# Kernel tuning notes

Hardware: AMD Instinct MI355X
Metric: run time of the kernel (lower is better)

The kernel has to match this reference:

```python
import jax, jax.numpy as jnp
import numpy as np

# Architecture constants pinned by the source script
D_MODEL = 2      # input_size / problemDim
ED = 64          # d_inner = expand_factor * d_model = hidden_size
N = 32           # d_state
K = 16           # d_conv
DT_RANK = 1      # ceil(d_model / 16)
NC = 4           # num_classes
B, L = 16, 2048


def setup_inputs() -> dict:
    key = jax.random.key(0)
    ks = jax.random.split(key, 16)
    rn = lambda k, shape, sc=0.1: jax.random.normal(k, shape, jnp.float32) * sc
    return {
        "x": jax.random.normal(ks[0], (B, L, D_MODEL), jnp.float32),
        "norm_w": jnp.ones((D_MODEL,), jnp.float32),
        "w_in": rn(ks[1], (D_MODEL, 2 * ED)),            # in_proj (no bias)
        "conv_w": rn(ks[2], (ED, 1, K)),                  # depthwise causal conv
        "conv_b": rn(ks[3], (ED,)),
        "w_xproj": rn(ks[4], (ED, DT_RANK + 2 * N)),      # x_proj (no bias)
        "w_dt": rn(ks[5], (DT_RANK, ED)),                 # dt_proj
        "b_dt": rn(ks[6], (ED,)),
        "A_log": jnp.log(jnp.tile(jnp.arange(1, N + 1, dtype=jnp.float32), (ED, 1))),
        "D_skip": jnp.ones((ED,), jnp.float32),
        "w_out": rn(ks[7], (ED, ED)),                     # out_proj (classifier mode: d_inner->d_inner)
        "b_out": rn(ks[8], (ED,)),
        "w_fc": rn(ks[9], (ED, ED)),
        "b_fc": rn(ks[10], (ED,)),
        "w_cls": rn(ks[11], (ED, NC)),
        "b_cls": rn(ks[12], (NC,)),
        "w_reg": rn(ks[13], (ED, 1)),
        "b_reg": rn(ks[14], (1,)),
    }


def _rmsnorm(x, w, eps=1e-5):
    return x * jax.lax.rsqrt(jnp.mean(x * x, axis=-1, keepdims=True) + eps) * w


def _silu(x):
    return x * jax.nn.sigmoid(x)


def reference(x, norm_w, w_in, conv_w, conv_b, w_xproj, w_dt, b_dt, A_log, D_skip,
              w_out, b_out, w_fc, b_fc, w_cls, b_cls, w_reg, b_reg):
    # --- Mamba block (n_layers = 1, classifier mode: no residual back to d_model) ---
    h = _rmsnorm(x, norm_w)                                # [B,L,D]
    xz = h @ w_in                                          # [B,L,2*ED]
    xb, z = jnp.split(xz, 2, axis=-1)
    # depthwise causal conv over time (torch pads K-1 both sides then slices [:L] == left-pad K-1)
    xc = jnp.transpose(xb, (0, 2, 1))                      # [B,ED,L]
    xc = jax.lax.conv_general_dilated(
        xc, conv_w, window_strides=(1,), padding=[(K - 1, 0)],
        feature_group_count=ED, dimension_numbers=("NCH", "OIH", "NCH"))
    xc = xc + conv_b[None, :, None]
    xb = _silu(jnp.transpose(xc, (0, 2, 1)))               # [B,L,ED]
    # input-dependent SSM parameters
    dbc = xb @ w_xproj                                     # [B,L,dt_rank+2N]
    delta = jax.nn.softplus(dbc[..., :DT_RANK] @ w_dt + b_dt)   # [B,L,ED]
    Bm = dbc[..., DT_RANK:DT_RANK + N]                     # [B,L,N]
    C = dbc[..., DT_RANK + N:]                             # [B,L,N]
    A = -jnp.exp(A_log)                                    # [ED,N]
    dA = jnp.exp(delta[..., None] * A)                     # [B,L,ED,N]
    dBx = delta[..., None] * Bm[:, :, None, :] * xb[..., None]  # [B,L,ED,N]

    # selective scan: h_t = dA_t * h_{t-1} + dBx_t ; y_t = <h_t, C_t>
    def step(hst, inp):
        dA_t, dBx_t, C_t = inp
        hst = dA_t * hst + dBx_t                           # [B,ED,N]
        y = jnp.einsum("ben,bn->be", hst, C_t)
        return hst, y

    h0 = jnp.zeros((x.shape[0], ED, N), x.dtype)
    xs = (jnp.transpose(dA, (1, 0, 2, 3)),
          jnp.transpose(dBx, (1, 0, 2, 3)),
          jnp.transpose(C, (1, 0, 2)))
    _, ys = jax.lax.scan(step, h0, xs)                     # [L,B,ED]
    y = jnp.transpose(ys, (1, 0, 2)) + D_skip * xb         # [B,L,ED]
    y = y * _silu(z)                                       # gate
    out = y @ w_out + b_out                                # [B,L,ED]

    last = out[:, -1, :]                                   # [B,ED]
    hs = jax.nn.relu(last @ w_fc + b_fc)
    class_logits = hs @ w_cls + b_cls                      # [B,NC]
    mass_pred = (hs @ w_reg + b_reg)[:, 0]                 # [B]
    return class_logits, mass_pred
```

## Files before the change

### kernel.cpp

```cpp
#include <hip/hip_runtime.h>
#include <math.h>

#define BB 16
#define LL 2048
#define ED 64
#define NN 32
#define KK 16
#define NCHUNK 64
#define CH 32
#define NBLK (BB * NCHUNK)
#define NSEG 4
#define CPS (NCHUNK / NSEG)

__global__ __launch_bounds__(256) void k1_featscan(
    const float* __restrict__ x, const float* __restrict__ norm_w,
    const float* __restrict__ w_in, const float* __restrict__ conv_w,
    const float* __restrict__ conv_b, const float* __restrict__ w_xproj,
    const float* __restrict__ w_dt, const float* __restrict__ b_dt,
    float* __restrict__ sbuf, float* __restrict__ dsumbuf,
    float* __restrict__ xlast, float* __restrict__ zl, float* __restrict__ cl)
{
    const int bx = blockIdx.x;
    const int b = bx >> 6, ti = bx & 63;
    const int l0 = ti * CH;
    const int tid = threadIdx.x;

    __shared__ float xbl[CH][ED + 1];
    __shared__ float hh[2 * (CH + KK - 1)];
    __shared__ float wdt[ED];
    __shared__ float wxs[ED][NN];
    __shared__ float dsp[4][ED];
    __shared__ __align__(16) union U {
        float pre[CH + KK - 1][ED];
        struct {
            float2 dlrl[CH][ED];
            float bml[CH][36];
            float dtr[CH];
        } sb;
    } u;

    for (int idx = tid; idx < ED * NN; idx += 256) {
        int e = idx >> 5, j = idx & 31;
        wxs[e][j] = w_xproj[e * 65 + 1 + j];
    }
    if (tid < ED) wdt[tid] = w_xproj[tid * 65];

    if (tid < 2 * (CH + KK - 1)) {
        int p = tid >> 1, c = tid & 1;
        int l = l0 - (KK - 1) + p;
        hh[tid] = (l >= 0) ? x[(b * LL + l) * 2 + c] : 0.f;
    }
    __syncthreads();
    if (tid < CH + KK - 1) {
        float x0 = hh[2 * tid], x1 = hh[2 * tid + 1];
        float s = rsqrtf(0.5f * (x0 * x0 + x1 * x1) + 1e-5f);
        hh[2 * tid]     = x0 * s * norm_w[0];
        hh[2 * tid + 1] = x1 * s * norm_w[1];
    }
    __syncthreads();
    {
        const int e = tid & 63;
        const float w0 = w_in[e], w1 = w_in[128 + e];
        for (int idx = tid; idx < (CH + KK - 1) * ED; idx += 256) {
            int p = idx >> 6;
            u.pre[p][e] = hh[2 * p] * w0 + hh[2 * p + 1] * w1;
        }
    }
    __syncthreads();
    {
        const int e = tid & 63, tg = tid >> 6, t0 = tg * 8;
        const float4 c0 = *(const float4*)(conv_w + e * KK);
        const float4 c1 = *(const float4*)(conv_w + e * KK + 4);
        const float4 c2 = *(const float4*)(conv_w + e * KK + 8);
        const float4 c3 = *(const float4*)(conv_w + e * KK + 12);
        const float cw[KK] = {c0.x, c0.y, c0.z, c0.w, c1.x, c1.y, c1.z, c1.w,
                              c2.x, c2.y, c2.z, c2.w, c3.x, c3.y, c3.z, c3.w};
        float w[8 + KK - 1];
        #pragma unroll
        for (int i = 0; i < 8 + KK - 1; ++i) w[i] = u.pre[t0 + i][e];
        const float bias = conv_b[e];
        #pragma unroll
        for (int i = 0; i < 8; ++i) {
            float acc = bias;
            #pragma unroll
            for (int k = 0; k < KK; ++k) acc = __fmaf_rn(cw[k], w[i + k], acc);
            xbl[t0 + i][e] = acc / (1.f + __expf(-acc));
        }
    }
    __syncthreads();
    {
        const int t = tid & 31, jg = tid >> 5;
        float a0 = 0.f, a1 = 0.f, a2 = 0.f, a3 = 0.f;
        for (int e = 0; e < ED; ++e) {
            float xv = xbl[t][e];
            const float4 wv = *(const float4*)&wxs[e][jg * 4];
            a0 = __fmaf_rn(xv, wv.x, a0);
            a1 = __fmaf_rn(xv, wv.y, a1);
            a2 = __fmaf_rn(xv, wv.z, a2);
            a3 = __fmaf_rn(xv, wv.w, a3);
        }
        u.sb.bml[t][jg * 4 + 0] = a0;
        u.sb.bml[t][jg * 4 + 1] = a1;
        u.sb.bml[t][jg * 4 + 2] = a2;
        u.sb.bml[t][jg * 4 + 3] = a3;
    }
    if (tid < CH) {
        float acc = 0.f;
        for (int e = 0; e < ED; ++e)
            acc = __fmaf_rn(xbl[tid][e], wdt[e], acc);
        u.sb.dtr[tid] = acc;
    }
    if (ti == NCHUNK - 1) {
        if (tid < NN) {
            float acc = 0.f;
            for (int e = 0; e < ED; ++e)
                acc = __fmaf_rn(xbl[CH - 1][e], w_xproj[e * 65 + 33 + tid], acc);
            cl[b * NN + tid] = acc;
        } else if (tid >= 64 && tid < 128) {
            int e = tid - 64;
            int pl = 2 * (CH + KK - 2);
            zl[b * ED + e] = hh[pl] * w_in[64 + e] + hh[pl + 1] * w_in[192 + e];
        } else if (tid >= 128 && tid < 192) {
            int e = tid - 128;
            xlast[b * ED + e] = xbl[CH - 1][e];
        }
    }
    __syncthreads();
    {
        const int e = tid & 63, tg = tid >> 6;
        const float wde = w_dt[e], bde = b_dt[e];
        float dpart = 0.f;
        #pragma unroll
        for (int k = 0; k < 8; ++k) {
            int s = tg + 4 * k;
            float v = __fmaf_rn(u.sb.dtr[s], wde, bde);
            float d = (v > 15.f) ? v : __logf(1.f + __expf(v));
            dpart += d;
            u.sb.dlrl[s][e] = make_float2(__expf(-d), d * xbl[s][e]);
        }
        dsp[tg][e] = dpart;
    }
    __syncthreads();
    {
        const int e = tid & 63, ng = tid >> 6, n0 = ng * 8;
        float S[8];
        #pragma unroll
        for (int j = 0; j < 8; ++j) S[j] = 0.f;

        for (int s = 0; s < CH; ++s) {
            const float2 rd = u.sb.dlrl[s][e];
            const float r = rd.x, dx = rd.y;
            const float4 b0 = *(const float4*)&u.sb.bml[s][n0];
            const float4 b1 = *(const float4*)&u.sb.bml[s][n0 + 4];
            float r2 = r * r, r4 = r2 * r2, r8 = r4 * r4;
            float bb1 = (ng & 1) ? r8 : 1.f;
            float bb2 = (ng & 2) ? r8 * r8 : 1.f;
            float m = r * bb1 * bb2;
            S[0] = __fmaf_rn(m, S[0], dx * b0.x); m *= r;
            S[1] = __fmaf_rn(m, S[1], dx * b0.y); m *= r;
            S[2] = __fmaf_rn(m, S[2], dx * b0.z); m *= r;
            S[3] = __fmaf_rn(m, S[3], dx * b0.w); m *= r;
            S[4] = __fmaf_rn(m, S[4], dx * b1.x); m *= r;
            S[5] = __fmaf_rn(m, S[5], dx * b1.y); m *= r;
            S[6] = __fmaf_rn(m, S[6], dx * b1.z); m *= r;
            S[7] = __fmaf_rn(m, S[7], dx * b1.w);
        }

        const int gbase = (ti * BB + b) * (ED * NN) + e * NN + n0;
        *(float4*)&sbuf[gbase]     = make_float4(S[0], S[1], S[2], S[3]);
        *(float4*)&sbuf[gbase + 4] = make_float4(S[4], S[5], S[6], S[7]);
        if (tid < 64) {
            float Dsum = dsp[0][tid] + dsp[1][tid] + dsp[2][tid] + dsp[3][tid];
            dsumbuf[(ti * BB + b) * ED + tid] = Dsum;
        }
    }
}

__global__ __launch_bounds__(256) void k2_fold(
    const float* __restrict__ sbuf, const float* __restrict__ dsumbuf,
    const float* __restrict__ A_log, float* __restrict__ hfin)
{
    const int tid = threadIdx.x;
    const int sid = tid & 63, seg = tid >> 6;
    const int state = blockIdx.x * 64 + sid;
    const int b = state >> 11, r = state & 2047;
    const int e = r >> 5, n = r & 31;
    const float A = -__expf(A_log[e * NN + n]);

    float M = 1.f, S = 0.f;
    const int c0 = seg * CPS;
    #pragma unroll
    for (int k = 0; k < CPS; ++k) {
        const int c = c0 + k;
        float m = __expf(A * dsumbuf[(c * BB + b) * ED + e]);
        S = __fmaf_rn(m, S, sbuf[(c * BB + b) * (ED * NN) + r]);
        M *= m;
    }

    __shared__ float Ms[NSEG][64], Ss[NSEG][64];
    Ms[seg][sid] = M;
    Ss[seg][sid] = S;
    __syncthreads();
    if (seg == 0) {
        float h = S;
        #pragma unroll
        for (int k = 1; k < NSEG; ++k)
            h = __fmaf_rn(Ms[k][sid], h, Ss[k][sid]);
        hfin[state] = h;
    }
}

__global__ __launch_bounds__(256) void k3_tail(
    const float* __restrict__ hfin, const float* __restrict__ cl,
    const float* __restrict__ zl, const float* __restrict__ xlast,
    const float* __restrict__ D_skip, const float* __restrict__ w_out,
    const float* __restrict__ b_out, const float* __restrict__ w_fc,
    const float* __restrict__ b_fc, const float* __restrict__ w_cls,
    const float* __restrict__ b_cls, const float* __restrict__ w_reg,
    const float* __restrict__ b_reg, float* __restrict__ out)
{
    const int b = blockIdx.x, tid = threadIdx.x;
    const int e = tid & 63, ng = tid >> 6, n0 = ng * 8;

    __shared__ float part[4][ED];
    __shared__ float ylds[ED], olds[ED], hlds[ED];

    float acc;
    {
        const float4 h0 = *(const float4*)&hfin[b * (ED * NN) + e * NN + n0];
        const float4 h1 = *(const float4*)&hfin[b * (ED * NN) + e * NN + n0 + 4];
        const float4 q0 = *(const float4*)&cl[b * NN + n0];
        const float4 q1 = *(const float4*)&cl[b * NN + n0 + 4];
        acc = h0.x * q0.x + h0.y * q0.y + h0.z * q0.z + h0.w * q0.w
            + h1.x * q1.x + h1.y * q1.y + h1.z * q1.z + h1.w * q1.w;
    }
    part[ng][e] = acc;
    __syncthreads();

    if (tid < ED) {
        float y = part[0][tid] + part[1][tid] + part[2][tid] + part[3][tid];
        y = __fmaf_rn(D_skip[tid], xlast[b * ED + tid], y);
        float z = zl[b * ED + tid];
        y *= z / (1.f + __expf(-z));
        ylds[tid] = y;
    }
    __syncthreads();

    if (tid < ED) {
        float a2 = b_out[tid];
        #pragma unroll 8
        for (int ee = 0; ee < ED; ++ee)
            a2 = __fmaf_rn(ylds[ee], w_out[ee * ED + tid], a2);
        olds[tid] = a2;
    }
    __syncthreads();

    if (tid < ED) {
        float a3 = b_fc[tid];
        #pragma unroll 8
        for (int ee = 0; ee < ED; ++ee)
            a3 = __fmaf_rn(olds[ee], w_fc[ee * ED + tid], a3);
        hlds[tid] = fmaxf(a3, 0.f);
    }
    __syncthreads();

    if (tid < 4) {
        float a4 = b_cls[tid];
        for (int ee = 0; ee < ED; ++ee)
            a4 = __fmaf_rn(hlds[ee], w_cls[ee * 4 + tid], a4);
        out[b * 4 + tid] = a4;
    } else if (tid == 4) {
        float a5 = b_reg[0];
        for (int ee = 0; ee < ED; ++ee)
            a5 = __fmaf_rn(hlds[ee], w_reg[ee], a5);
        out[BB * 4 + b] = a5;
    }
}

extern "C" void kernel_launch(void* const* d_in, const int* in_sizes, int n_in,
                              void* d_out, int out_size, void* d_ws, size_t ws_size,
                              hipStream_t stream) {
    const float* x       = (const float*)d_in[0];
    const float* norm_w  = (const float*)d_in[1];
    const float* w_in    = (const float*)d_in[2];
    const float* conv_w  = (const float*)d_in[3];
    const float* conv_b  = (const float*)d_in[4];
    const float* w_xproj = (const float*)d_in[5];
    const float* w_dt    = (const float*)d_in[6];
    const float* b_dt    = (const float*)d_in[7];
    const float* A_log   = (const float*)d_in[8];
    const float* D_skip  = (const float*)d_in[9];
    const float* w_out   = (const float*)d_in[10];
    const float* b_out   = (const float*)d_in[11];
    const float* w_fc    = (const float*)d_in[12];
    const float* b_fc    = (const float*)d_in[13];
    const float* w_cls   = (const float*)d_in[14];
    const float* b_cls   = (const float*)d_in[15];
    const float* w_reg   = (const float*)d_in[16];
    const float* b_reg   = (const float*)d_in[17];
    float* out = (float*)d_out;

    float* ws      = (float*)d_ws;
    float* sbuf    = ws;
    float* dsumbuf = sbuf + NCHUNK * BB * ED * NN;
    float* hfin    = dsumbuf + NCHUNK * BB * ED;
    float* xlast   = hfin + BB * ED * NN;
    float* zl      = xlast + BB * ED;
    float* cl      = zl + BB * ED;

    k1_featscan<<<NBLK, 256, 0, stream>>>(x, norm_w, w_in, conv_w, conv_b,
                                          w_xproj, w_dt, b_dt,
                                          sbuf, dsumbuf, xlast, zl, cl);
    k2_fold<<<(BB * ED * NN * NSEG) / 256, 256, 0, stream>>>(sbuf, dsumbuf,
                                                             A_log, hfin);
    k3_tail<<<BB, 256, 0, stream>>>(hfin, cl, zl, xlast, D_skip,
                                    w_out, b_out, w_fc, b_fc,
                                    w_cls, b_cls, w_reg, b_reg, out);
}
```

Measured before the change: 116.3 us.

## Broadcast x_proj B values via readlane instead of a shared-memory staging buffer

The B-projection results stay in registers and are broadcast to the scan loop with wave readlane, instead of being written to a shared-memory bml array and read back. This removes an LDS round trip and shrinks the shared-memory union by overlaying the wxs weights with the conv pre-buffer. The x_proj and dt dot products now read shared memory as float4, with xbl padded to 68 floats per row so those loads stay aligned. A launch-bounds occupancy hint of 4 blocks is added. The trade-off is more scalar readlane instructions in the inner scan loop and possible register pressure from the occupancy hint.

```diff
diff --git a/kernel.cpp b/kernel.cpp
--- a/kernel.cpp
+++ b/kernel.cpp
@@ -11,8 +11,13 @@
 #define NBLK (BB * NCHUNK)
 #define NSEG 4
 #define CPS (NCHUNK / NSEG)
-
-__global__ __launch_bounds__(256) void k1_featscan(
+#define XS (ED + 4)
+
+__device__ __forceinline__ float rlane(float v, int l) {
+    return __uint_as_float(__builtin_amdgcn_readlane(__float_as_uint(v), l));
+}
+
+__global__ __launch_bounds__(256, 4) void k1_featscan(
     const float* __restrict__ x, const float* __restrict__ norm_w,
     const float* __restrict__ w_in, const float* __restrict__ conv_w,
     const float* __restrict__ conv_b, const float* __restrict__ w_xproj,
@@ -25,23 +30,24 @@
     const int l0 = ti * CH;
     const int tid = threadIdx.x;
 
-    __shared__ float xbl[CH][ED + 1];
+    __shared__ __align__(16) float xbl[CH][XS];
     __shared__ float hh[2 * (CH + KK - 1)];
-    __shared__ float wdt[ED];
-    __shared__ float wxs[ED][NN];
+    __shared__ __align__(16) float wdt[ED];
     __shared__ float dsp[4][ED];
     __shared__ __align__(16) union U {
-        float pre[CH + KK - 1][ED];
         struct {
+            float pre[CH + KK - 1][ED];
+            float wxs[ED][NN];
+        } a;
+        struct {
+            float dtr[CH];
             float2 dlrl[CH][ED];
-            float bml[CH][36];
-            float dtr[CH];
-        } sb;
+        } b;
     } u;
 
     for (int idx = tid; idx < ED * NN; idx += 256) {
         int e = idx >> 5, j = idx & 31;
-        wxs[e][j] = w_xproj[e * 65 + 1 + j];
+        u.a.wxs[e][j] = w_xproj[e * 65 + 1 + j];
     }
     if (tid < ED) wdt[tid] = w_xproj[tid * 65];
 
@@ -63,7 +69,7 @@
         const float w0 = w_in[e], w1 = w_in[128 + e];
         for (int idx = tid; idx < (CH + KK - 1) * ED; idx += 256) {
             int p = idx >> 6;
-            u.pre[p][e] = hh[2 * p] * w0 + hh[2 * p + 1] * w1;
+            u.a.pre[p][e] = hh[2 * p] * w0 + hh[2 * p + 1] * w1;
         }
     }
     __syncthreads();
@@ -77,7 +83,7 @@
                               c2.x, c2.y, c2.z, c2.w, c3.x, c3.y, c3.z, c3.w};
         float w[8 + KK - 1];
         #pragma unroll
-        for (int i = 0; i < 8 + KK - 1; ++i) w[i] = u.pre[t0 + i][e];
+        for (int i = 0; i < 8 + KK - 1; ++i) w[i] = u.a.pre[t0 + i][e];
         const float bias = conv_b[e];
         #pragma unroll
         for (int i = 0; i < 8; ++i) {
@@ -88,27 +94,36 @@
         }
     }
     __syncthreads();
+    float a0 = 0.f, a1 = 0.f, a2 = 0.f, a3 = 0.f;
     {
         const int t = tid & 31, jg = tid >> 5;
-        float a0 = 0.f, a1 = 0.f, a2 = 0.f, a3 = 0.f;
-        for (int e = 0; e < ED; ++e) {
-            float xv = xbl[t][e];
-            const float4 wv = *(const float4*)&wxs[e][jg * 4];
-            a0 = __fmaf_rn(xv, wv.x, a0);
-            a1 = __fmaf_rn(xv, wv.y, a1);
-            a2 = __fmaf_rn(xv, wv.z, a2);
-            a3 = __fmaf_rn(xv, wv.w, a3);
-        }
-        u.sb.bml[t][jg * 4 + 0] = a0;
-        u.sb.bml[t][jg * 4 + 1] = a1;
-        u.sb.bml[t][jg * 4 + 2] = a2;
-        u.sb.bml[t][jg * 4 + 3] = a3;
+        for (int e = 0; e < ED; e += 4) {
+            const float4 xv = *(const float4*)&xbl[t][e];
+            const float4 w0 = *(const float4*)&u.a.wxs[e + 0][jg * 4];
+            const float4 w1 = *(const float4*)&u.a.wxs[e + 1][jg * 4];
+            const float4 w2 = *(const float4*)&u.a.wxs[e + 2][jg * 4];
+            const float4 w3 = *(const float4*)&u.a.wxs[e + 3][jg * 4];
+            a0 = __fmaf_rn(xv.x, w0.x, a0); a1 = __fmaf_rn(xv.x, w0.y, a1);
+            a2 = __fmaf_rn(xv.x, w0.z, a2); a3 = __fmaf_rn(xv.x, w0.w, a3);
+            a0 = __fmaf_rn(xv.y, w1.x, a0); a1 = __fmaf_rn(xv.y, w1.y, a1);
+            a2 = __fmaf_rn(xv.y, w1.z, a2); a3 = __fmaf_rn(xv.y, w1.w, a3);
+            a0 = __fmaf_rn(xv.z, w2.x, a0); a1 = __fmaf_rn(xv.z, w2.y, a1);
+            a2 = __fmaf_rn(xv.z, w2.z, a2); a3 = __fmaf_rn(xv.z, w2.w, a3);
+            a0 = __fmaf_rn(xv.w, w3.x, a0); a1 = __fmaf_rn(xv.w, w3.y, a1);
+            a2 = __fmaf_rn(xv.w, w3.z, a2); a3 = __fmaf_rn(xv.w, w3.w, a3);
+        }
     }
     if (tid < CH) {
         float acc = 0.f;
-        for (int e = 0; e < ED; ++e)
-            acc = __fmaf_rn(xbl[tid][e], wdt[e], acc);
-        u.sb.dtr[tid] = acc;
+        for (int e = 0; e < ED; e += 4) {
+            const float4 xv = *(const float4*)&xbl[tid][e];
+            const float4 wv = *(const float4*)&wdt[e];
+            acc = __fmaf_rn(xv.x, wv.x, acc);
+            acc = __fmaf_rn(xv.y, wv.y, acc);
+            acc = __fmaf_rn(xv.z, wv.z, acc);
+            acc = __fmaf_rn(xv.w, wv.w, acc);
+        }
+        u.b.dtr[tid] = acc;
     }
     if (ti == NCHUNK - 1) {
         if (tid < NN) {
@@ -133,10 +148,10 @@
         #pragma unroll
         for (int k = 0; k < 8; ++k) {
             int s = tg + 4 * k;
-            float v = __fmaf_rn(u.sb.dtr[s], wde, bde);
+            float v = __fmaf_rn(u.b.dtr[s], wde, bde);
             float d = (v > 15.f) ? v : __logf(1.f + __expf(v));
             dpart += d;
-            u.sb.dlrl[s][e] = make_float2(__expf(-d), d * xbl[s][e]);
+            u.b.dlrl[s][e] = make_float2(__expf(-d), d * xbl[s][e]);
         }
         dsp[tg][e] = dpart;
     }
@@ -148,22 +163,24 @@
         for (int j = 0; j < 8; ++j) S[j] = 0.f;
 
         for (int s = 0; s < CH; ++s) {
-            const float2 rd = u.sb.dlrl[s][e];
+            const float2 rd = u.b.dlrl[s][e];
             const float r = rd.x, dx = rd.y;
-            const float4 b0 = *(const float4*)&u.sb.bml[s][n0];
-            const float4 b1 = *(const float4*)&u.sb.bml[s][n0 + 4];
+            const float b0x = rlane(a0, s),      b0y = rlane(a1, s);
+            const float b0z = rlane(a2, s),      b0w = rlane(a3, s);
+            const float b1x = rlane(a0, s + 32), b1y = rlane(a1, s + 32);
+            const float b1z = rlane(a2, s + 32), b1w = rlane(a3, s + 32);
             float r2 = r * r, r4 = r2 * r2, r8 = r4 * r4;
             float bb1 = (ng & 1) ? r8 : 1.f;
             float bb2 = (ng & 2) ? r8 * r8 : 1.f;
             float m = r * bb1 * bb2;
-            S[0] = __fmaf_rn(m, S[0], dx * b0.x); m *= r;
-            S[1] = __fmaf_rn(m, S[1], dx * b0.y); m *= r;
-            S[2] = __fmaf_rn(m, S[2], dx * b0.z); m *= r;
-            S[3] = __fmaf_rn(m, S[3], dx * b0.w); m *= r;
-            S[4] = __fmaf_rn(m, S[4], dx * b1.x); m *= r;
-            S[5] = __fmaf_rn(m, S[5], dx * b1.y); m *= r;
-            S[6] = __fmaf_rn(m, S[6], dx * b1.z); m *= r;
-            S[7] = __fmaf_rn(m, S[7], dx * b1.w);
+            S[0] = __fmaf_rn(m, S[0], dx * b0x); m *= r;
+            S[1] = __fmaf_rn(m, S[1], dx * b0y); m *= r;
+            S[2] = __fmaf_rn(m, S[2], dx * b0z); m *= r;
+            S[3] = __fmaf_rn(m, S[3], dx * b0w); m *= r;
+            S[4] = __fmaf_rn(m, S[4], dx * b1x); m *= r;
+            S[5] = __fmaf_rn(m, S[5], dx * b1y); m *= r;
+            S[6] = __fmaf_rn(m, S[6], dx * b1z); m *= r;
+            S[7] = __fmaf_rn(m, S[7], dx * b1w);
         }
 
         const int gbase = (ti * BB + b) * (ED * NN) + e * NN + n0;
```

Measured after the change: 214.2 us. +84.1%, slower.
